# Performance work log

Hardware: AMD Instinct MI355X
Metric: run time of the kernel (lower is better)

## Reference

```python
import jax, jax.numpy as jnp
import numpy as np

SCENE = (256, 256, 32)   # scene_size
SCALE = 2                # project_scale
EPS = 1e-8               # torch cosine_similarity eps


def _per_view(src_flat, idx, mask):
    # src_flat: [c, H*W]; idx: [N, P] int; mask: [N, P] bool
    c, hw = src_flat.shape
    # append zero column so out-of-fov indices gather zeros (torch: cat zeros_vec)
    src = jnp.concatenate([src_flat, jnp.zeros((c, 1), src_flat.dtype)], axis=1)
    idx = jnp.where(mask, idx, hw)          # invalid -> zero column h*w
    gathered = src[:, idx]                  # [c, N, P]
    feat_sum = gathered.sum(-1)             # [c, N] (sum over patterns)
    cnt = mask.astype(src.dtype).sum(-1)    # [N] valid-pattern count
    valid = cnt > 0
    # feat_sum/cnt with NaN(0/0)->0, done divide-safely (identical values)
    feat = jnp.where(valid, feat_sum / jnp.where(valid, cnt, 1.0), 0.0)
    w = valid.astype(src.dtype)             # cnt/cnt with NaN->0
    return feat, w


def sfa_forward(x2d, projected_pix, fov_mask):
    v, c, h, w = x2d.shape
    n = projected_pix.shape[1]
    idx = projected_pix[..., 1] * w + projected_pix[..., 0]      # [V, N, P]
    feats, wts = jax.vmap(_per_view)(x2d.reshape(v, c, h * w), idx, fov_mask)
    # feats: [V, c, N]; wts: [V, N]
    acc = jnp.zeros((c, n), x2d.dtype)
    for i in range(v):
        for j in range(i + 1, v):
            fi, fj = feats[i], feats[j]
            dot = jnp.sum(fi * fj, axis=0)                       # [N]
            nsq = jnp.sum(fi * fi, axis=0) * jnp.sum(fj * fj, axis=0)
            # dot / max(||fi||*||fj||, eps), grad-safe form
            cos = dot * jax.lax.rsqrt(jnp.maximum(nsq, EPS * EPS))
            wij = wts[i] * wts[j]
            diff = wts[i] - wts[j]
            wi = (diff > 0).astype(x2d.dtype)
            wj = (diff < 0).astype(x2d.dtype)
            cw = cos * wij
            acc = acc + (cw + wi) * fi + (cw + wj) * fj
    out = acc / (v * (v - 1)) if v > 1 else feats[0]
    sx, sy, sz = SCENE[0] // SCALE, SCENE[1] // SCALE, SCENE[2] // SCALE
    return out.reshape(c, sx, sy, sz)   # kitti layout


def setup_inputs() -> dict:
    V, C, H, W = 2, 64, 128, 416
    N, P = 262144, 4
    key = jax.random.key(0)
    k1, k2, k3, k4 = jax.random.split(key, 4)
    x2d = jax.random.normal(k1, (V, C, H, W), dtype=jnp.float32)
    pix_x = jax.random.randint(k2, (V, N, P), 0, W)
    pix_y = jax.random.randint(k3, (V, N, P), 0, H)
    projected_pix = jnp.stack([pix_x, pix_y], axis=-1)           # [V, N, P, 2]
    fov_mask = jax.random.uniform(k4, (V, N, P)) < 0.7
    return {"x2d": x2d, "projected_pix": projected_pix, "fov_mask": fov_mask}


def reference(x2d, projected_pix, fov_mask):
    return sfa_forward(x2d, projected_pix, fov_mask)
```

## Files before the change

### kernel.cpp

```cpp
#include <hip/hip_runtime.h>
#include <hip/hip_fp16.h>

#define NV 2
#define NC 64
#define NH 128
#define NW 416
#define NHW (NH * NW)
#define NPT 262144
#define HWBLK (NHW / 64)

__global__ void sfa_detect(const unsigned char* __restrict__ mask,
                           int* __restrict__ flag) {
    __shared__ int cnt;
    if (threadIdx.x == 0) cnt = 0;
    __syncthreads();
    int local = 0;
    for (int i = threadIdx.x; i < 1024; i += 256)
        if ((i & 3) != 0 && mask[i] != 0) local++;
    if (local) atomicAdd(&cnt, local);
    __syncthreads();
    if (threadIdx.x == 0) flag[0] = (cnt > 8) ? 1 : 0;
}

__global__ __launch_bounds__(256) void sfa_transpose(const float* __restrict__ x2d,
                                                     __half* __restrict__ xT) {
    __shared__ float tile[64][68];
    const int b = blockIdx.x;
    const int v = b / HWBLK;
    const int hw0 = (b % HWBLK) * 64;
    const int t = threadIdx.x;
    const int l16 = t & 15;
    const int g = t >> 4;

    const float* src = x2d + (size_t)v * NC * NHW;
#pragma unroll
    for (int k = 0; k < 4; ++k) {
        int c = g + 16 * k;
        float4 val = *(const float4*)(src + (size_t)c * NHW + hw0 + l16 * 4);
        *(float4*)&tile[c][l16 * 4] = val;
    }
    __syncthreads();
    uint2* dst = (uint2*)(xT + ((size_t)v * NHW + hw0) * NC);
#pragma unroll
    for (int k = 0; k < 4; ++k) {
        int j = g + 16 * k;
        int c = l16 * 4;
        __half2 h01 = __floats2half2_rn(tile[c + 0][j], tile[c + 1][j]);
        __half2 h23 = __floats2half2_rn(tile[c + 2][j], tile[c + 3][j]);
        uint2 o;
        o.x = *(unsigned*)&h01;
        o.y = *(unsigned*)&h23;
        dst[(size_t)j * 16 + l16] = o;
    }
}

__global__ __launch_bounds__(256) void sfa_main2(const unsigned* __restrict__ xT,
                                                 const int* __restrict__ pix,
                                                 const unsigned char* __restrict__ maskb,
                                                 const int* __restrict__ flagp,
                                                 float* __restrict__ out) {
    __shared__ float tile[64][68];
    const int byteMask = flagp[0];
    const int t = threadIdx.x;
    const int lane = t & 63;
    const int l = lane & 31;
    const int g = lane >> 5;
    const int wv = t >> 6;
    const int n0 = blockIdx.x * 64;

#pragma unroll 2
    for (int i = 0; i < 8; ++i) {
        const int pt = (wv << 4) + (i << 1) + g;
        const int n = n0 + pt;
        float2 f[2];
        int cv[2];
#pragma unroll
        for (int v = 0; v < 2; ++v) {
            const int4* pp = (const int4*)(pix + (((size_t)v * NPT + n) << 3));
            int4 a = pp[0];
            int4 b = pp[1];
            unsigned i0 = (unsigned)(a.y * NW + a.x);
            unsigned i1 = (unsigned)(a.w * NW + a.z);
            unsigned i2 = (unsigned)(b.y * NW + b.x);
            unsigned i3 = (unsigned)(b.w * NW + b.z);
            int m0, m1, m2, m3;
            size_t moff = ((size_t)v * NPT + n) << 2;
            if (byteMask) {
                uchar4 m = *(const uchar4*)(maskb + moff);
                m0 = m.x; m1 = m.y; m2 = m.z; m3 = m.w;
            } else {
                int4 m = *(const int4*)((const int*)maskb + moff);
                m0 = m.x; m1 = m.y; m2 = m.z; m3 = m.w;
            }
            const unsigned* bu = xT + ((size_t)v * NHW) * 32u;
            unsigned u0 = bu[(i0 << 5) + l];
            unsigned u1 = bu[(i1 << 5) + l];
            unsigned u2 = bu[(i2 << 5) + l];
            unsigned u3 = bu[(i3 << 5) + l];
            u0 = m0 ? u0 : 0u;
            u1 = m1 ? u1 : 0u;
            u2 = m2 ? u2 : 0u;
            u3 = m3 ? u3 : 0u;
            __half2 s = __hadd2(__hadd2(*(__half2*)&u0, *(__half2*)&u1),
                                __hadd2(*(__half2*)&u2, *(__half2*)&u3));
            int c = (m0 ? 1 : 0) + (m1 ? 1 : 0) + (m2 ? 1 : 0) + (m3 ? 1 : 0);
            float rcp = (c == 0) ? 0.f
                      : (c == 1) ? 1.f
                      : (c == 2) ? 0.5f
                      : (c == 3) ? (1.f / 3.f)
                                 : 0.25f;
            float2 sf = __half22float2(s);
            f[v].x = sf.x * rcp;
            f[v].y = sf.y * rcp;
            cv[v] = c;
        }
        float2 f0 = f[0], f1 = f[1];
        float d  = f0.x * f1.x + f0.y * f1.y;
        float q0 = f0.x * f0.x + f0.y * f0.y;
        float q1 = f1.x * f1.x + f1.y * f1.y;
#pragma unroll
        for (int m = 1; m < 32; m <<= 1) {
            d  += __shfl_xor(d, m, 64);
            q0 += __shfl_xor(q0, m, 64);
            q1 += __shfl_xor(q1, m, 64);
        }
        float cosv = d * rsqrtf(fmaxf(q0 * q1, 1e-16f));
        float w0 = cv[0] > 0 ? 1.f : 0.f;
        float w1 = cv[1] > 0 ? 1.f : 0.f;
        float cw = cosv * w0 * w1;
        float wi = (w0 > w1) ? 1.f : 0.f;
        float wj = (w1 > w0) ? 1.f : 0.f;
        float ox = ((cw + wi) * f0.x + (cw + wj) * f1.x) * 0.5f;
        float oy = ((cw + wi) * f0.y + (cw + wj) * f1.y) * 0.5f;
        tile[2 * l + 0][pt] = ox;
        tile[2 * l + 1][pt] = oy;
    }
    __syncthreads();
    const int c = t >> 2;
    const int jb = (t & 3) << 4;
    float* op = out + (size_t)c * NPT + n0 + jb;
#pragma unroll
    for (int k = 0; k < 4; ++k) {
        float4 o4 = *(const float4*)&tile[c][jb + (k << 2)];
        *(float4*)(op + (k << 2)) = o4;
    }
}

__global__ __launch_bounds__(256) void sfa_main_fb(const float* __restrict__ src,
                                                   const int* __restrict__ pix,
                                                   const unsigned char* __restrict__ maskb,
                                                   const int* __restrict__ flagp,
                                                   float* __restrict__ out) {
    __shared__ float tile[64][68];
    const int byteMask = flagp[0];
    const int t = threadIdx.x;
    const int lane = t & 63;
    const int wv = t >> 6;
    const int n0 = blockIdx.x * 64;

    for (int i = 0; i < 16; ++i) {
        const int pt = (wv << 4) + i;
        const int n = n0 + pt;
        float fv[2];
        int cv[2];
#pragma unroll
        for (int v = 0; v < 2; ++v) {
            const int4* pp = (const int4*)(pix + (((size_t)v * NPT + n) << 3));
            int4 a = pp[0];
            int4 b = pp[1];
            int i0 = a.y * NW + a.x;
            int i1 = a.w * NW + a.z;
            int i2 = b.y * NW + b.x;
            int i3 = b.w * NW + b.z;
            int m0, m1, m2, m3;
            size_t moff = ((size_t)v * NPT + n) << 2;
            if (byteMask) {
                uchar4 m = *(const uchar4*)(maskb + moff);
                m0 = m.x; m1 = m.y; m2 = m.z; m3 = m.w;
            } else {
                int4 m = *(const int4*)((const int*)maskb + moff);
                m0 = m.x; m1 = m.y; m2 = m.z; m3 = m.w;
            }
            const float* base = src + (size_t)(v * NC + lane) * NHW;
            float v0 = base[i0], v1 = base[i1], v2 = base[i2], v3 = base[i3];
            float s = (m0 ? v0 : 0.f) + (m1 ? v1 : 0.f) +
                      (m2 ? v2 : 0.f) + (m3 ? v3 : 0.f);
            int c = (m0 ? 1 : 0) + (m1 ? 1 : 0) + (m2 ? 1 : 0) + (m3 ? 1 : 0);
            float rcp = (c == 0) ? 0.f
                      : (c == 1) ? 1.f
                      : (c == 2) ? 0.5f
                      : (c == 3) ? (1.f / 3.f)
                                 : 0.25f;
            fv[v] = s * rcp;
            cv[v] = c;
        }
        float f0 = fv[0], f1 = fv[1];
        float d = f0 * f1, q0 = f0 * f0, q1 = f1 * f1;
#pragma unroll
        for (int m = 1; m < 64; m <<= 1) {
            d  += __shfl_xor(d, m, 64);
            q0 += __shfl_xor(q0, m, 64);
            q1 += __shfl_xor(q1, m, 64);
        }
        float cosv = d * rsqrtf(fmaxf(q0 * q1, 1e-16f));
        float w0 = cv[0] > 0 ? 1.f : 0.f;
        float w1 = cv[1] > 0 ? 1.f : 0.f;
        float cw = cosv * w0 * w1;
        float wi = (w0 > w1) ? 1.f : 0.f;
        float wj = (w1 > w0) ? 1.f : 0.f;
        float o = ((cw + wi) * f0 + (cw + wj) * f1) * 0.5f;
        tile[lane][pt] = o;
    }
    __syncthreads();
    const int c = t >> 2;
    const int jb = (t & 3) << 4;
    float* op = out + (size_t)c * NPT + n0 + jb;
#pragma unroll
    for (int k = 0; k < 4; ++k) {
        float4 o4 = *(const float4*)&tile[c][jb + (k << 2)];
        *(float4*)(op + (k << 2)) = o4;
    }
}

extern "C" void kernel_launch(void* const* d_in, const int* in_sizes, int n_in,
                              void* d_out, int out_size, void* d_ws, size_t ws_size,
                              hipStream_t stream) {
    const float* x2d = (const float*)d_in[0];
    const int* pix = (const int*)d_in[1];
    const unsigned char* mask = (const unsigned char*)d_in[2];
    float* out = (float*)d_out;

    int* flag = (int*)d_ws;
    __half* xT = (__half*)((char*)d_ws + 256);
    const size_t need = 256 + (size_t)NV * NHW * NC * sizeof(__half);

    sfa_detect<<<1, 256, 0, stream>>>(mask, flag);
    if (ws_size >= need) {
        sfa_transpose<<<NV * HWBLK, 256, 0, stream>>>(x2d, xT);
        sfa_main2<<<NPT / 64, 256, 0, stream>>>((const unsigned*)xT, pix, mask,
                                                flag, out);
    } else {
        sfa_main_fb<<<NPT / 64, 256, 0, stream>>>(x2d, pix, mask, flag, out);
    }
}
```

Measured before the change: 73.84 us.

## Gather 16-byte channel chunks per lane with a shorter shuffle reduction

The main kernel now has 8 lanes per point, and each lane loads a uint4 (8 half channels) per pattern, replacing 32 lanes each loading 4 bytes. This cuts the number of gather instructions and shrinks the cross-lane reduction from 5 xor steps to 3 by doing more of the dot and norm sums in registers. The shared-memory output tile drops its padding and uses a rotated (skewed) index to avoid bank conflicts. In exchange, each lane uses more registers, and each 128-byte row is fetched as wider per-lane loads.

```diff
diff --git a/kernel.cpp b/kernel.cpp
--- a/kernel.cpp
+++ b/kernel.cpp
@@ -54,25 +54,30 @@
     }
 }
 
-__global__ __launch_bounds__(256) void sfa_main2(const unsigned* __restrict__ xT,
+static __device__ __forceinline__ unsigned hadd2u(unsigned a, unsigned b) {
+    __half2 r = __hadd2(*(const __half2*)&a, *(const __half2*)&b);
+    return *(unsigned*)&r;
+}
+
+__global__ __launch_bounds__(256) void sfa_main3(const unsigned* __restrict__ xT,
                                                  const int* __restrict__ pix,
                                                  const unsigned char* __restrict__ maskb,
                                                  const int* __restrict__ flagp,
                                                  float* __restrict__ out) {
-    __shared__ float tile[64][68];
+    __shared__ float tile[64 * 64];
     const int byteMask = flagp[0];
     const int t = threadIdx.x;
     const int lane = t & 63;
-    const int l = lane & 31;
-    const int g = lane >> 5;
+    const int q = lane & 7;
+    const int p = lane >> 3;
     const int wv = t >> 6;
     const int n0 = blockIdx.x * 64;
 
-#pragma unroll 2
-    for (int i = 0; i < 8; ++i) {
-        const int pt = (wv << 4) + (i << 1) + g;
+#pragma unroll
+    for (int i = 0; i < 2; ++i) {
+        const int pt = (wv << 4) + (i << 3) + p;
         const int n = n0 + pt;
-        float2 f[2];
+        float f[2][8];
         int cv[2];
 #pragma unroll
         for (int v = 0; v < 2; ++v) {
@@ -92,34 +97,48 @@
                 int4 m = *(const int4*)((const int*)maskb + moff);
                 m0 = m.x; m1 = m.y; m2 = m.z; m3 = m.w;
             }
-            const unsigned* bu = xT + ((size_t)v * NHW) * 32u;
-            unsigned u0 = bu[(i0 << 5) + l];
-            unsigned u1 = bu[(i1 << 5) + l];
-            unsigned u2 = bu[(i2 << 5) + l];
-            unsigned u3 = bu[(i3 << 5) + l];
-            u0 = m0 ? u0 : 0u;
-            u1 = m1 ? u1 : 0u;
-            u2 = m2 ? u2 : 0u;
-            u3 = m3 ? u3 : 0u;
-            __half2 s = __hadd2(__hadd2(*(__half2*)&u0, *(__half2*)&u1),
-                                __hadd2(*(__half2*)&u2, *(__half2*)&u3));
+            const unsigned* bu = xT + (((size_t)v * NHW) << 5) + (q << 2);
+            uint4 u0 = *(const uint4*)(bu + ((size_t)i0 << 5));
+            uint4 u1 = *(const uint4*)(bu + ((size_t)i1 << 5));
+            uint4 u2 = *(const uint4*)(bu + ((size_t)i2 << 5));
+            uint4 u3 = *(const uint4*)(bu + ((size_t)i3 << 5));
+            u0.x = m0 ? u0.x : 0u; u0.y = m0 ? u0.y : 0u;
+            u0.z = m0 ? u0.z : 0u; u0.w = m0 ? u0.w : 0u;
+            u1.x = m1 ? u1.x : 0u; u1.y = m1 ? u1.y : 0u;
+            u1.z = m1 ? u1.z : 0u; u1.w = m1 ? u1.w : 0u;
+            u2.x = m2 ? u2.x : 0u; u2.y = m2 ? u2.y : 0u;
+            u2.z = m2 ? u2.z : 0u; u2.w = m2 ? u2.w : 0u;
+            u3.x = m3 ? u3.x : 0u; u3.y = m3 ? u3.y : 0u;
+            u3.z = m3 ? u3.z : 0u; u3.w = m3 ? u3.w : 0u;
+            unsigned s0 = hadd2u(hadd2u(u0.x, u1.x), hadd2u(u2.x, u3.x));
+            unsigned s1 = hadd2u(hadd2u(u0.y, u1.y), hadd2u(u2.y, u3.y));
+            unsigned s2 = hadd2u(hadd2u(u0.z, u1.z), hadd2u(u2.z, u3.z));
+            unsigned s3 = hadd2u(hadd2u(u0.w, u1.w), hadd2u(u2.w, u3.w));
             int c = (m0 ? 1 : 0) + (m1 ? 1 : 0) + (m2 ? 1 : 0) + (m3 ? 1 : 0);
             float rcp = (c == 0) ? 0.f
                       : (c == 1) ? 1.f
                       : (c == 2) ? 0.5f
                       : (c == 3) ? (1.f / 3.f)
                                  : 0.25f;
-            float2 sf = __half22float2(s);
-            f[v].x = sf.x * rcp;
-            f[v].y = sf.y * rcp;
+            float2 f01 = __half22float2(*(const __half2*)&s0);
+            float2 f23 = __half22float2(*(const __half2*)&s1);
+            float2 f45 = __half22float2(*(const __half2*)&s2);
+            float2 f67 = __half22float2(*(const __half2*)&s3);
+            f[v][0] = f01.x * rcp; f[v][1] = f01.y * rcp;
+            f[v][2] = f23.x * rcp; f[v][3] = f23.y * rcp;
+            f[v][4] = f45.x * rcp; f[v][5] = f45.y * rcp;
+            f[v][6] = f67.x * rcp; f[v][7] = f67.y * rcp;
             cv[v] = c;
         }
-        float2 f0 = f[0], f1 = f[1];
-        float d  = f0.x * f1.x + f0.y * f1.y;
-        float q0 = f0.x * f0.x + f0.y * f0.y;
-        float q1 = f1.x * f1.x + f1.y * f1.y;
-#pragma unroll
-        for (int m = 1; m < 32; m <<= 1) {
+        float d = 0.f, q0 = 0.f, q1 = 0.f;
+#pragma unroll
+        for (int j = 0; j < 8; ++j) {
+            d  = fmaf(f[0][j], f[1][j], d);
+            q0 = fmaf(f[0][j], f[0][j], q0);
+            q1 = fmaf(f[1][j], f[1][j], q1);
+        }
+#pragma unroll
+        for (int m = 1; m < 8; m <<= 1) {
             d  += __shfl_xor(d, m, 64);
             q0 += __shfl_xor(q0, m, 64);
             q1 += __shfl_xor(q1, m, 64);
@@ -130,10 +149,13 @@
         float cw = cosv * w0 * w1;
         float wi = (w0 > w1) ? 1.f : 0.f;
         float wj = (w1 > w0) ? 1.f : 0.f;
-        float ox = ((cw + wi) * f0.x + (cw + wj) * f1.x) * 0.5f;
-        float oy = ((cw + wi) * f0.y + (cw + wj) * f1.y) * 0.5f;
-        tile[2 * l + 0][pt] = ox;
-        tile[2 * l + 1][pt] = oy;
+        float cw0 = (cw + wi) * 0.5f;
+        float cw1 = (cw + wj) * 0.5f;
+#pragma unroll
+        for (int j = 0; j < 8; ++j) {
+            int row = (q << 3) + j;
+            tile[(row << 6) + ((pt + row) & 63)] = cw0 * f[0][j] + cw1 * f[1][j];
+        }
     }
     __syncthreads();
     const int c = t >> 2;
@@ -141,7 +163,11 @@
     float* op = out + (size_t)c * NPT + n0 + jb;
 #pragma unroll
     for (int k = 0; k < 4; ++k) {
-        float4 o4 = *(const float4*)&tile[c][jb + (k << 2)];
+        float4 o4;
+        o4.x = tile[(c << 6) + ((jb + (k << 2) + 0 + c) & 63)];
+        o4.y = tile[(c << 6) + ((jb + (k << 2) + 1 + c) & 63)];
+        o4.z = tile[(c << 6) + ((jb + (k << 2) + 2 + c) & 63)];
+        o4.w = tile[(c << 6) + ((jb + (k << 2) + 3 + c) & 63)];
         *(float4*)(op + (k << 2)) = o4;
     }
 }
@@ -237,7 +263,7 @@
     sfa_detect<<<1, 256, 0, stream>>>(mask, flag);
     if (ws_size >= need) {
         sfa_transpose<<<NV * HWBLK, 256, 0, stream>>>(x2d, xT);
-        sfa_main2<<<NPT / 64, 256, 0, stream>>>((const unsigned*)xT, pix, mask,
+        sfa_main3<<<NPT / 64, 256, 0, stream>>>((const unsigned*)xT, pix, mask,
                                                 flag, out);
     } else {
         sfa_main_fb<<<NPT / 64, 256, 0, stream>>>(x2d, pix, mask, flag, out);
```

Measured after the change: 67.43 us. -8.7%, faster.
